# Kernel optimization log

Measured on AMD Instinct MI355X. Metric: run time of the kernel, lower is better.

## Reference

```python
import jax, jax.numpy as jnp
import numpy as np

B, T, F = 8, 4096, 256

def setup_inputs() -> dict:
    key = jax.random.key(0)
    ks = jax.random.split(key, 10)
    s = 1.0 / np.sqrt(F)
    return {
        "x": jax.random.normal(ks[0], (B, T, F), dtype=jnp.float32),
        "Wq_w": jax.random.normal(ks[1], (F, F), dtype=jnp.float32) * s,
        "Wq_b": jax.random.normal(ks[2], (F,), dtype=jnp.float32) * 0.01,
        "Wk_w": jax.random.normal(ks[3], (F, F), dtype=jnp.float32) * s,
        "Wk_b": jax.random.normal(ks[4], (F,), dtype=jnp.float32) * 0.01,
        "Wv_w": jax.random.normal(ks[5], (F, F), dtype=jnp.float32) * s,
        "Wv_b": jax.random.normal(ks[6], (F,), dtype=jnp.float32) * 0.01,
        "w": jax.random.normal(ks[7], (T, T), dtype=jnp.float32) * 0.02,
        "out_w": jax.random.normal(ks[8], (F, F), dtype=jnp.float32) * s,
        "out_b": jax.random.normal(ks[9], (F,), dtype=jnp.float32) * 0.01,
    }

def reference(x, Wq_w, Wq_b, Wk_w, Wk_b, Wv_w, Wv_b, w, out_w, out_b):
    # Linear layers (torch convention: y = x @ W.T + b)
    Q = x @ Wq_w.T + Wq_b                      # [B, T, F]
    K = x @ Wk_w.T + Wk_b                      # [B, T, F]
    V = x @ Wv_w.T + Wv_b                      # [B, T, F]
    Q_sig = jax.nn.sigmoid(Q)
    # Stabilized exponentials (faithful: w over rows, K over FEATURE dim)
    exp_w = jnp.exp(w - jnp.max(w, axis=-1, keepdims=True))        # [T, T]
    exp_K = jnp.exp(K - jnp.max(K, axis=-1, keepdims=True))        # [B, T, F]
    num = jnp.einsum('ts,bsf->btf', exp_w, exp_K * V)              # [B, T, F]
    den = jnp.einsum('ts,bsf->btf', exp_w, exp_K)                  # [B, T, F]
    Yt = Q_sig * (num / den)
    return Yt @ out_w.T + out_b
```

## Files before the change

### kernel.cpp

```cpp
#include <hip/hip_runtime.h>
#include <hip/hip_bf16.h>

#define BB 8
#define TT 4096
#define FF 256
#define BT 32768

typedef unsigned short u16;
typedef __attribute__((ext_vector_type(8))) short short8;
typedef __attribute__((ext_vector_type(4))) float f32x4;
typedef __attribute__((ext_vector_type(4))) unsigned int u32x4;

static __device__ __forceinline__ float bf2f(u16 u) {
    union { unsigned int i; float f; } v; v.i = ((unsigned int)u) << 16; return v.f;
}
static __device__ __forceinline__ u16 f2bf(float f) {
    union { float f; unsigned int i; } v; v.f = f;
    unsigned int x = v.i;
    return (u16)((x + 0x7fffu + ((x >> 16) & 1u)) >> 16);
}

typedef const __attribute__((address_space(1))) void gvoid_t;
typedef __attribute__((address_space(3))) void svoid_t;

__global__ __launch_bounds__(256) void expw_kernel(const float* __restrict__ w,
                                                   u16* __restrict__ ew) {
    __shared__ float red[256];
    int row = blockIdx.x;
    int tid = threadIdx.x;
    const float* wr = w + (size_t)row * TT;

    f32x4 vals[4];
    float m = -1e30f;
#pragma unroll
    for (int v = 0; v < 4; ++v) {
        int idx = (v * 256 + tid) * 4;
        vals[v] = *(const f32x4*)(wr + idx);
#pragma unroll
        for (int j = 0; j < 4; ++j) m = fmaxf(m, vals[v][j]);
    }
    red[tid] = m;
    __syncthreads();
    for (int s = 128; s > 0; s >>= 1) {
        if (tid < s) red[tid] = fmaxf(red[tid], red[tid + s]);
        __syncthreads();
    }
    float rm = red[0];
#pragma unroll
    for (int v = 0; v < 4; ++v) {
        int idx = (v * 256 + tid) * 4;
        float e0 = expf(vals[v][0] - rm), e1 = expf(vals[v][1] - rm);
        float e2 = expf(vals[v][2] - rm), e3 = expf(vals[v][3] - rm);
        uint2 pk;
        pk.x = (unsigned int)f2bf(e0) | ((unsigned int)f2bf(e1) << 16);
        pk.y = (unsigned int)f2bf(e2) | ((unsigned int)f2bf(e3) << 16);
        *(uint2*)(ew + (size_t)row * TT + idx) = pk;
    }
}

__global__ __launch_bounds__(256) void cvt_all_kernel(const float* __restrict__ x,
                                                      const float* __restrict__ wq,
                                                      const float* __restrict__ wo,
                                                      const float* __restrict__ wk,
                                                      const float* __restrict__ wv,
                                                      u16* __restrict__ xbf,
                                                      u16* __restrict__ wqb,
                                                      u16* __restrict__ wob,
                                                      u16* __restrict__ wkv) {
    int i = blockIdx.x * 256 + threadIdx.x;
    if (i < 2097152) {
        int idx = i * 4;
        f32x4 v = *(const f32x4*)(x + idx);
        uint2 pk;
        pk.x = (unsigned int)f2bf(v[0]) | ((unsigned int)f2bf(v[1]) << 16);
        pk.y = (unsigned int)f2bf(v[2]) | ((unsigned int)f2bf(v[3]) << 16);
        *(uint2*)(xbf + idx) = pk;
        return;
    }
    int j = i - 2097152;
    int which = j >> 14, k = j & 16383;
    int idx = k * 4;
    if (which == 0) {
        f32x4 v = *(const f32x4*)(wq + idx);
        uint2 pk;
        pk.x = (unsigned int)f2bf(v[0]) | ((unsigned int)f2bf(v[1]) << 16);
        pk.y = (unsigned int)f2bf(v[2]) | ((unsigned int)f2bf(v[3]) << 16);
        *(uint2*)(wqb + idx) = pk;
    } else if (which == 1) {
        f32x4 v = *(const f32x4*)(wo + idx);
        uint2 pk;
        pk.x = (unsigned int)f2bf(v[0]) | ((unsigned int)f2bf(v[1]) << 16);
        pk.y = (unsigned int)f2bf(v[2]) | ((unsigned int)f2bf(v[3]) << 16);
        *(uint2*)(wob + idx) = pk;
    } else {
        int f = idx >> 8, c = idx & 255;
        f32x4 a = *(const f32x4*)(wk + idx);
        f32x4 b = *(const f32x4*)(wv + idx);
        uint2 pa, pb;
        pa.x = (unsigned int)f2bf(a[0]) | ((unsigned int)f2bf(a[1]) << 16);
        pa.y = (unsigned int)f2bf(a[2]) | ((unsigned int)f2bf(a[3]) << 16);
        pb.x = (unsigned int)f2bf(b[0]) | ((unsigned int)f2bf(b[1]) << 16);
        pb.y = (unsigned int)f2bf(b[2]) | ((unsigned int)f2bf(b[3]) << 16);
        *(uint2*)(wkv + (size_t)(2 * f) * 256 + c) = pa;
        *(uint2*)(wkv + (size_t)(2 * f + 1) * 256 + c) = pb;
    }
}

template <int MODE>
__global__ __launch_bounds__(256) void gemm_nt(const u16* __restrict__ A,
                                               const u16* __restrict__ Bm,
                                               const float* __restrict__ bias,
                                               void* __restrict__ Call,
                                               int M, int N, int K) {
    __shared__ u16 As[128 * 32];
    __shared__ u16 Bs[128 * 32];

    int tid = threadIdx.x;
    int lane = tid & 63;
    int w = tid >> 6;
    int wr = w >> 1, wc = w & 1;
    int fr = lane & 15, kg = lane >> 4;

    f32x4 acc[4][4];
#pragma unroll
    for (int m = 0; m < 4; ++m)
#pragma unroll
        for (int n = 0; n < 4; ++n) acc[m][n] = (f32x4){0.f, 0.f, 0.f, 0.f};

    int bm = blockIdx.x, bn = blockIdx.y;
    int nk = K >> 5;

    int srow = tid >> 2;
    int schunk = ((tid & 3) ^ ((tid >> 3) & 3)) << 3;
    const u16* aBase = A + (size_t)(bm * 128 + srow) * K + schunk;
    const u16* bBase = Bm + (size_t)(bn * 128 + srow) * K + schunk;
    size_t half = (size_t)64 * K;

    int xsw = (kg * 8) ^ (((fr >> 1) & 3) << 3);

    for (int kt = 0; kt < nk; ++kt) {
        __syncthreads();
        int ko = kt << 5;
        __builtin_amdgcn_global_load_lds((gvoid_t*)(aBase + ko), (svoid_t*)&As[tid * 8], 16, 0, 0);
        __builtin_amdgcn_global_load_lds((gvoid_t*)(aBase + half + ko), (svoid_t*)&As[2048 + tid * 8], 16, 0, 0);
        __builtin_amdgcn_global_load_lds((gvoid_t*)(bBase + ko), (svoid_t*)&Bs[tid * 8], 16, 0, 0);
        __builtin_amdgcn_global_load_lds((gvoid_t*)(bBase + half + ko), (svoid_t*)&Bs[2048 + tid * 8], 16, 0, 0);
        __syncthreads();

        short8 af[4], bfr[4];
#pragma unroll
        for (int m = 0; m < 4; ++m)
            af[m] = *(const short8*)&As[(wr * 64 + m * 16 + fr) * 32 + xsw];
#pragma unroll
        for (int n = 0; n < 4; ++n)
            bfr[n] = *(const short8*)&Bs[(wc * 64 + n * 16 + fr) * 32 + xsw];
#pragma unroll
        for (int m = 0; m < 4; ++m)
#pragma unroll
            for (int n = 0; n < 4; ++n)
                acc[m][n] = __builtin_amdgcn_mfma_f32_16x16x32_bf16(af[m], bfr[n], acc[m][n], 0, 0, 0);
    }

    int row0 = bm * 128 + wr * 64;
    int col0 = bn * 128 + wc * 64;
#pragma unroll
    for (int n = 0; n < 4; ++n) {
        int col = col0 + n * 16 + fr;
        float bv = bias ? bias[col] : 0.0f;
#pragma unroll
        for (int m = 0; m < 4; ++m) {
            int rbase = row0 + m * 16 + kg * 4;
#pragma unroll
            for (int i = 0; i < 4; ++i) {
                float val = acc[m][n][i] + bv;
                size_t idx = (size_t)(rbase + i) * N + col;
                if (MODE == 0)
                    ((float*)Call)[idx] = val;
                else
                    ((u16*)Call)[idx] = f2bf(1.0f / (1.0f + expf(-val)));
            }
        }
    }
}

__global__ __launch_bounds__(512) void kv_mt_kernel(const u16* __restrict__ xbf,
                                                    const u16* __restrict__ wkv,
                                                    const float* __restrict__ bk,
                                                    const float* __restrict__ bv,
                                                    u16* __restrict__ mt) {
    __shared__ u16 As[128 * 32];
    __shared__ u16 Bs[512 * 32];
    __shared__ float rmax4[128][4];

    int tid = threadIdx.x;
    int lane = tid & 63, wid = tid >> 6;
    int fr = lane & 15, kg = lane >> 4;
    int wr = wid >> 2, wc = wid & 3;
    int row0g = blockIdx.x * 128;

    f32x4 acc[4][8];
#pragma unroll
    for (int m = 0; m < 4; ++m)
#pragma unroll
        for (int n = 0; n < 8; ++n) acc[m][n] = (f32x4){0.f, 0.f, 0.f, 0.f};

    int scol = ((tid & 3) ^ ((tid >> 3) & 3)) << 3;
    const u16* aSrc = xbf + (size_t)(row0g + (tid >> 2)) * 256 + scol;
    const u16* bSrc = wkv + (size_t)(tid >> 2) * 256 + scol;
    int xsw = (kg * 8) ^ (((fr >> 1) & 3) << 3);

    for (int ks = 0; ks < 8; ++ks) {
        __syncthreads();
        __builtin_amdgcn_global_load_lds((gvoid_t*)(aSrc + ks * 32), (svoid_t*)&As[tid * 8], 16, 0, 0);
#pragma unroll
        for (int c = 0; c < 4; ++c)
            __builtin_amdgcn_global_load_lds((gvoid_t*)(bSrc + (size_t)c * 128 * 256 + ks * 32),
                                             (svoid_t*)&Bs[c * 4096 + tid * 8], 16, 0, 0);
        __syncthreads();

        short8 af[4], bfr[8];
#pragma unroll
        for (int m = 0; m < 4; ++m)
            af[m] = *(const short8*)&As[(wr * 64 + m * 16 + fr) * 32 + xsw];
#pragma unroll
        for (int n = 0; n < 8; ++n)
            bfr[n] = *(const short8*)&Bs[(wc * 128 + n * 16 + fr) * 32 + xsw];
#pragma unroll
        for (int m = 0; m < 4; ++m)
#pragma unroll
            for (int n = 0; n < 8; ++n)
                acc[m][n] = __builtin_amdgcn_mfma_f32_16x16x32_bf16(af[m], bfr[n], acc[m][n], 0, 0, 0);
    }

    int par = fr & 1;
#pragma unroll
    for (int n = 0; n < 8; ++n) {
        int col = wc * 128 + n * 16 + fr;
        int f = col >> 1;
        float bvv = par ? bv[f] : bk[f];
#pragma unroll
        for (int m = 0; m < 4; ++m)
#pragma unroll
            for (int i = 0; i < 4; ++i) acc[m][n][i] += bvv;
    }

    float rmax[4][4];
#pragma unroll
    for (int m = 0; m < 4; ++m)
#pragma unroll
        for (int i = 0; i < 4; ++i) {
            float mx = -1e30f;
#pragma unroll
            for (int n = 0; n < 8; ++n) mx = fmaxf(mx, par ? -1e30f : acc[m][n][i]);
            mx = fmaxf(mx, __shfl_xor(mx, 2));
            mx = fmaxf(mx, __shfl_xor(mx, 4));
            mx = fmaxf(mx, __shfl_xor(mx, 8));
            mx = fmaxf(mx, __shfl_xor(mx, 1));
            rmax[m][i] = mx;
        }
    if (fr == 0) {
#pragma unroll
        for (int m = 0; m < 4; ++m)
#pragma unroll
            for (int i = 0; i < 4; ++i)
                rmax4[wr * 64 + m * 16 + kg * 4 + i][wc] = rmax[m][i];
    }
    __syncthreads();
#pragma unroll
    for (int m = 0; m < 4; ++m)
#pragma unroll
        for (int i = 0; i < 4; ++i) {
            f32x4 r4 = *(const f32x4*)rmax4[wr * 64 + m * 16 + kg * 4 + i];
            rmax[m][i] = fmaxf(fmaxf(r4[0], r4[1]), fmaxf(r4[2], r4[3]));
        }

    int b = row0g >> 12;
    int tcb = (row0g & 4095) + wr * 64;
#pragma unroll
    for (int n = 0; n < 8; ++n) {
        int col = wc * 128 + n * 16 + fr;
        int f = col >> 1;
        size_t rowmt = (size_t)(b * 512 + 2 * f + (par ? 0 : 1));
#pragma unroll
        for (int m = 0; m < 4; ++m) {
            int tc = tcb + m * 16 + kg * 4;
            u16 o[4];
#pragma unroll
            for (int i = 0; i < 4; ++i) {
                float v = acc[m][n][i];
                float ek = expf(v - rmax[m][i]);
                float ekx = __shfl_xor(ek, 1);
                float outv = par ? (ekx * v) : ek;
                o[i] = f2bf(outv);
            }
            uint2 pk;
            pk.x = (unsigned int)o[0] | ((unsigned int)o[1] << 16);
            pk.y = (unsigned int)o[2] | ((unsigned int)o[3] << 16);
            *(uint2*)(mt + rowmt * TT + tc) = pk;
        }
    }
}

#define GLDS(src, eoff) \
    __builtin_amdgcn_global_load_lds((gvoid_t*)(src), (svoid_t*)&L[eoff], 16, 0, 0)

#define STAGE8(P_, KS_) do {                                                   \
    _Pragma("unroll")                                                          \
    for (int i_ = 0; i_ < 4; ++i_) {                                           \
        GLDS(sA + (size_t)i_ * 64 * 4096 + (KS_) * 64,                         \
             (P_) * 16384 + i_ * 4096 + dst);                                  \
        GLDS(sB + (size_t)i_ * 64 * 4096 + (KS_) * 64,                         \
             32768 + (P_) * 16384 + i_ * 4096 + dst);                          \
    }                                                                          \
} while (0)

__global__ __launch_bounds__(512, 2) void gemm256_nt(const u16* __restrict__ A,
                                                     const u16* __restrict__ B,
                                                     const u16* __restrict__ qsig,
                                                     u16* __restrict__ yt) {
    __shared__ u16 L[65536];
    const int K = 4096;
    int tid = threadIdx.x;
    int lane = tid & 63, wid = tid >> 6;
    int fr = lane & 15, kg = lane >> 4;
    int wr = wid >> 2, wc = wid & 3;
    int bm = blockIdx.x, bn = blockIdx.y;
    const char* LB = (const char*)L;

    int x0 = (kg * 16) ^ ((fr & 7) << 4);
    int x1 = (64 + kg * 16) ^ ((fr & 7) << 4);
    int arow = (wr * 128 + fr) * 128;
    int brow = (wc * 64 + fr) * 128;

    int scol = ((tid & 7) * 8) ^ (((tid >> 3) & 7) << 3);
    const u16* sA = A + (size_t)(bm * 256 + (tid >> 3)) * K + scol;
    const u16* sB = B + (size_t)(bn * 256 + (tid >> 3)) * K + scol;
    int dst = tid * 8;

    f32x4 acc[8][4];
#pragma unroll
    for (int m = 0; m < 8; ++m)
#pragma unroll
        for (int n = 0; n < 4; ++n) acc[m][n] = (f32x4){0.f, 0.f, 0.f, 0.f};

    STAGE8(0, 0);
    asm volatile("s_waitcnt vmcnt(0)" ::: "memory");
    __builtin_amdgcn_sched_barrier(0);
    __builtin_amdgcn_s_barrier();

#pragma unroll 1
    for (int t = 0; t < 64; ++t) {
        int p = t & 1;
        const char* abase = LB + p * 32768;
        const char* bbase = LB + 65536 + p * 32768;

        short8 bfr[4][2], af[4][2];
#pragma unroll
        for (int nf = 0; nf < 4; ++nf) {
            const char* rb = bbase + brow + nf * 2048;
            bfr[nf][0] = *(const short8*)(rb + x0);
            bfr[nf][1] = *(const short8*)(rb + x1);
        }
#pragma unroll
        for (int mf = 0; mf < 4; ++mf) {
            const char* rb = abase + arow + mf * 2048;
            af[mf][0] = *(const short8*)(rb + x0);
            af[mf][1] = *(const short8*)(rb + x1);
        }
        int ks = (t + 1 < 64) ? t + 1 : 0;
        STAGE8(p ^ 1, ks);
        asm volatile("s_waitcnt lgkmcnt(0)" ::: "memory");
        __builtin_amdgcn_sched_barrier(0);
        __builtin_amdgcn_s_setprio(1);
#pragma unroll
        for (int mf = 0; mf < 4; ++mf)
#pragma unroll
            for (int nf = 0; nf < 4; ++nf) {
                acc[mf][nf] = __builtin_amdgcn_mfma_f32_16x16x32_bf16(af[mf][0], bfr[nf][0], acc[mf][nf], 0, 0, 0);
                acc[mf][nf] = __builtin_amdgcn_mfma_f32_16x16x32_bf16(af[mf][1], bfr[nf][1], acc[mf][nf], 0, 0, 0);
            }
        __builtin_amdgcn_s_setprio(0);
#pragma unroll
        for (int mf = 0; mf < 4; ++mf) {
            const char* rb = abase + arow + (mf + 4) * 2048;
            af[mf][0] = *(const short8*)(rb + x0);
            af[mf][1] = *(const short8*)(rb + x1);
        }
        asm volatile("s_waitcnt lgkmcnt(0)" ::: "memory");
        __builtin_amdgcn_sched_barrier(0);
        __builtin_amdgcn_s_setprio(1);
#pragma unroll
        for (int mf = 0; mf < 4; ++mf)
#pragma unroll
            for (int nf = 0; nf < 4; ++nf) {
                acc[mf + 4][nf] = __builtin_amdgcn_mfma_f32_16x16x32_bf16(af[mf][0], bfr[nf][0], acc[mf + 4][nf], 0, 0, 0);
                acc[mf + 4][nf] = __builtin_amdgcn_mfma_f32_16x16x32_bf16(af[mf][1], bfr[nf][1], acc[mf + 4][nf], 0, 0, 0);
            }
        __builtin_amdgcn_s_setprio(0);
        asm volatile("s_waitcnt vmcnt(0)" ::: "memory");
        __builtin_amdgcn_sched_barrier(0);
        __builtin_amdgcn_s_barrier();
    }

    int colgb = bn * 256 + wc * 64;
    int row0 = bm * 256 + wr * 128;
    int par = fr & 1;
#pragma unroll
    for (int n = 0; n < 4; ++n) {
        int colg = colgb + n * 16 + fr;
        int b = colg >> 9;
        int f = (colg & 511) >> 1;
#pragma unroll
        for (int m = 0; m < 8; ++m) {
            int tr0 = row0 + m * 16 + kg * 4;
            float v0 = acc[m][n][0], v1 = acc[m][n][1];
            float v2 = acc[m][n][2], v3 = acc[m][n][3];
            float o0 = __shfl_xor(v0, 1), o1 = __shfl_xor(v1, 1);
            float o2 = __shfl_xor(v2, 1), o3 = __shfl_xor(v3, 1);
            float nA = par ? o2 : v0, dA = par ? v2 : o0;
            float nB = par ? o3 : v1, dB = par ? v3 : o1;
            int iA = par ? 2 : 0;
            size_t idxA = ((size_t)(b * 4096 + tr0 + iA) << 8) + f;
            size_t idxB = idxA + 256;
            float qA = bf2f(qsig[idxA]);
            float qB = bf2f(qsig[idxB]);
            yt[idxA] = f2bf(qA * nA * __builtin_amdgcn_rcpf(dA));
            yt[idxB] = f2bf(qB * nB * __builtin_amdgcn_rcpf(dB));
        }
    }
}

extern "C" void kernel_launch(void* const* d_in, const int* in_sizes, int n_in,
                              void* d_out, int out_size, void* d_ws, size_t ws_size,
                              hipStream_t stream) {
    const float* x  = (const float*)d_in[0];
    const float* wq = (const float*)d_in[1];
    const float* bq = (const float*)d_in[2];
    const float* wk = (const float*)d_in[3];
    const float* bk = (const float*)d_in[4];
    const float* wv = (const float*)d_in[5];
    const float* bv = (const float*)d_in[6];
    const float* w  = (const float*)d_in[7];
    const float* wo = (const float*)d_in[8];
    const float* bo = (const float*)d_in[9];

    char* p = (char*)d_ws;
    u16* expw = (u16*)p; p += (size_t)TT * TT * 2;
    u16* xbf  = (u16*)p; p += (size_t)BT * FF * 2;
    u16* wqb  = (u16*)p; p += (size_t)FF * FF * 2;
    u16* wob  = (u16*)p; p += (size_t)FF * FF * 2;
    u16* wkv  = (u16*)p; p += (size_t)2 * FF * FF * 2;
    u16* qsig = (u16*)p; p += (size_t)BT * FF * 2;
    u16* mt   = (u16*)p; p += (size_t)BB * 512 * TT * 2;
    u16* yt = xbf;

    expw_kernel<<<TT, 256, 0, stream>>>(w, expw);

    cvt_all_kernel<<<8384, 256, 0, stream>>>(x, wq, wo, wk, wv, xbf, wqb, wob, wkv);

    dim3 gp(BT / 128, FF / 128, 1);
    gemm_nt<1><<<gp, 256, 0, stream>>>(xbf, wqb, bq, qsig, BT, FF, FF);

    kv_mt_kernel<<<BT / 128, 512, 0, stream>>>(xbf, wkv, bk, bv, mt);

    gemm256_nt<<<dim3(16, 16), 512, 0, stream>>>(expw, mt, qsig, yt);

    gemm_nt<0><<<gp, 256, 0, stream>>>(yt, wob, bo, (float*)d_out, BT, FF, FF);
}
```

Measured before the change: 186.3 us.

## Shrink attention GEMM tile to 256x128 with K-step 32 and drop exp_w row max

The big exp_w × M GEMM now uses 256x128 output tiles with a 32-wide K step and a 48 KB LDS footprint. It declares 4 blocks per CU and launches twice as many blocks, aiming for more resident waves and better latency hiding. The price is half as many MFMAs per LDS fragment load and twice as many loop barriers. Separately, the exp(w) kernel no longer subtracts the row max, which cancels in the num/den ratio, so the reduction and its syncs are gone; this can overflow if w holds large values.

```diff
diff --git a/kernel.cpp b/kernel.cpp
--- a/kernel.cpp
+++ b/kernel.cpp
@@ -25,32 +25,15 @@
 
 __global__ __launch_bounds__(256) void expw_kernel(const float* __restrict__ w,
                                                    u16* __restrict__ ew) {
-    __shared__ float red[256];
     int row = blockIdx.x;
     int tid = threadIdx.x;
     const float* wr = w + (size_t)row * TT;
-
-    f32x4 vals[4];
-    float m = -1e30f;
 #pragma unroll
     for (int v = 0; v < 4; ++v) {
         int idx = (v * 256 + tid) * 4;
-        vals[v] = *(const f32x4*)(wr + idx);
-#pragma unroll
-        for (int j = 0; j < 4; ++j) m = fmaxf(m, vals[v][j]);
-    }
-    red[tid] = m;
-    __syncthreads();
-    for (int s = 128; s > 0; s >>= 1) {
-        if (tid < s) red[tid] = fmaxf(red[tid], red[tid + s]);
-        __syncthreads();
-    }
-    float rm = red[0];
-#pragma unroll
-    for (int v = 0; v < 4; ++v) {
-        int idx = (v * 256 + tid) * 4;
-        float e0 = expf(vals[v][0] - rm), e1 = expf(vals[v][1] - rm);
-        float e2 = expf(vals[v][2] - rm), e3 = expf(vals[v][3] - rm);
+        f32x4 vals = *(const f32x4*)(wr + idx);
+        float e0 = expf(vals[0]), e1 = expf(vals[1]);
+        float e2 = expf(vals[2]), e3 = expf(vals[3]);
         uint2 pk;
         pk.x = (unsigned int)f2bf(e0) | ((unsigned int)f2bf(e1) << 16);
         pk.y = (unsigned int)f2bf(e2) | ((unsigned int)f2bf(e3) << 16);
@@ -304,109 +287,90 @@
 #define GLDS(src, eoff) \
     __builtin_amdgcn_global_load_lds((gvoid_t*)(src), (svoid_t*)&L[eoff], 16, 0, 0)
 
-#define STAGE8(P_, KS_) do {                                                   \
-    _Pragma("unroll")                                                          \
-    for (int i_ = 0; i_ < 4; ++i_) {                                           \
-        GLDS(sA + (size_t)i_ * 64 * 4096 + (KS_) * 64,                         \
-             (P_) * 16384 + i_ * 4096 + dst);                                  \
-        GLDS(sB + (size_t)i_ * 64 * 4096 + (KS_) * 64,                         \
-             32768 + (P_) * 16384 + i_ * 4096 + dst);                          \
-    }                                                                          \
+#define STAGE3(P_, KS_) do {                                                   \
+    GLDS(sA + (KS_) * 32, (P_) * 8192 + dst);                                  \
+    GLDS(sA + (size_t)128 * 4096 + (KS_) * 32, (P_) * 8192 + 4096 + dst);      \
+    GLDS(sB + (KS_) * 32, 16384 + (P_) * 4096 + dst);                          \
 } while (0)
 
-__global__ __launch_bounds__(512, 2) void gemm256_nt(const u16* __restrict__ A,
+__global__ __launch_bounds__(512, 4) void gemm256_nt(const u16* __restrict__ A,
                                                      const u16* __restrict__ B,
                                                      const u16* __restrict__ qsig,
                                                      u16* __restrict__ yt) {
-    __shared__ u16 L[65536];
+    __shared__ u16 L[24576];
     const int K = 4096;
     int tid = threadIdx.x;
     int lane = tid & 63, wid = tid >> 6;
     int fr = lane & 15, kg = lane >> 4;
     int wr = wid >> 2, wc = wid & 3;
     int bm = blockIdx.x, bn = blockIdx.y;
-    const char* LB = (const char*)L;
-
-    int x0 = (kg * 16) ^ ((fr & 7) << 4);
-    int x1 = (64 + kg * 16) ^ ((fr & 7) << 4);
-    int arow = (wr * 128 + fr) * 128;
-    int brow = (wc * 64 + fr) * 128;
-
-    int scol = ((tid & 7) * 8) ^ (((tid >> 3) & 7) << 3);
-    const u16* sA = A + (size_t)(bm * 256 + (tid >> 3)) * K + scol;
-    const u16* sB = B + (size_t)(bn * 256 + (tid >> 3)) * K + scol;
+
+    int xsw = (kg * 8) ^ (((fr >> 1) & 3) << 3);
+    int arow = (wr * 128 + fr) * 32;
+    int brow = (wc * 32 + fr) * 32;
+
+    int scol = ((tid & 3) ^ ((tid >> 3) & 3)) << 3;
+    const u16* sA = A + (size_t)(bm * 256 + (tid >> 2)) * K + scol;
+    const u16* sB = B + (size_t)(bn * 128 + (tid >> 2)) * K + scol;
     int dst = tid * 8;
 
-    f32x4 acc[8][4];
+    f32x4 acc[8][2];
 #pragma unroll
     for (int m = 0; m < 8; ++m)
 #pragma unroll
-        for (int n = 0; n < 4; ++n) acc[m][n] = (f32x4){0.f, 0.f, 0.f, 0.f};
-
-    STAGE8(0, 0);
+        for (int n = 0; n < 2; ++n) acc[m][n] = (f32x4){0.f, 0.f, 0.f, 0.f};
+
+    STAGE3(0, 0);
     asm volatile("s_waitcnt vmcnt(0)" ::: "memory");
     __builtin_amdgcn_sched_barrier(0);
     __builtin_amdgcn_s_barrier();
 
 #pragma unroll 1
-    for (int t = 0; t < 64; ++t) {
+    for (int t = 0; t < 128; ++t) {
         int p = t & 1;
-        const char* abase = LB + p * 32768;
-        const char* bbase = LB + 65536 + p * 32768;
-
-        short8 bfr[4][2], af[4][2];
-#pragma unroll
-        for (int nf = 0; nf < 4; ++nf) {
-            const char* rb = bbase + brow + nf * 2048;
-            bfr[nf][0] = *(const short8*)(rb + x0);
-            bfr[nf][1] = *(const short8*)(rb + x1);
-        }
-#pragma unroll
-        for (int mf = 0; mf < 4; ++mf) {
-            const char* rb = abase + arow + mf * 2048;
-            af[mf][0] = *(const short8*)(rb + x0);
-            af[mf][1] = *(const short8*)(rb + x1);
-        }
-        int ks = (t + 1 < 64) ? t + 1 : 0;
-        STAGE8(p ^ 1, ks);
+        int Ab = p * 8192;
+        int Bb = 16384 + p * 4096;
+
+        short8 af[4], bfr[2];
+#pragma unroll
+        for (int nf = 0; nf < 2; ++nf)
+            bfr[nf] = *(const short8*)&L[Bb + brow + nf * 512 + xsw];
+#pragma unroll
+        for (int mf = 0; mf < 4; ++mf)
+            af[mf] = *(const short8*)&L[Ab + arow + mf * 512 + xsw];
+        int ks = (t + 1 < 128) ? t + 1 : 0;
+        STAGE3(p ^ 1, ks);
         asm volatile("s_waitcnt lgkmcnt(0)" ::: "memory");
         __builtin_amdgcn_sched_barrier(0);
         __builtin_amdgcn_s_setprio(1);
 #pragma unroll
         for (int mf = 0; mf < 4; ++mf)
 #pragma unroll
-            for (int nf = 0; nf < 4; ++nf) {
-                acc[mf][nf] = __builtin_amdgcn_mfma_f32_16x16x32_bf16(af[mf][0], bfr[nf][0], acc[mf][nf], 0, 0, 0);
-                acc[mf][nf] = __builtin_amdgcn_mfma_f32_16x16x32_bf16(af[mf][1], bfr[nf][1], acc[mf][nf], 0, 0, 0);
-            }
+            for (int nf = 0; nf < 2; ++nf)
+                acc[mf][nf] = __builtin_amdgcn_mfma_f32_16x16x32_bf16(af[mf], bfr[nf], acc[mf][nf], 0, 0, 0);
         __builtin_amdgcn_s_setprio(0);
 #pragma unroll
-        for (int mf = 0; mf < 4; ++mf) {
-            const char* rb = abase + arow + (mf + 4) * 2048;
-            af[mf][0] = *(const short8*)(rb + x0);
-            af[mf][1] = *(const short8*)(rb + x1);
-        }
+        for (int mf = 0; mf < 4; ++mf)
+            af[mf] = *(const short8*)&L[Ab + arow + (mf + 4) * 512 + xsw];
         asm volatile("s_waitcnt lgkmcnt(0)" ::: "memory");
         __builtin_amdgcn_sched_barrier(0);
         __builtin_amdgcn_s_setprio(1);
 #pragma unroll
         for (int mf = 0; mf < 4; ++mf)
 #pragma unroll
-            for (int nf = 0; nf < 4; ++nf) {
-                acc[mf + 4][nf] = __builtin_amdgcn_mfma_f32_16x16x32_bf16(af[mf][0], bfr[nf][0], acc[mf + 4][nf], 0, 0, 0);
-                acc[mf + 4][nf] = __builtin_amdgcn_mfma_f32_16x16x32_bf16(af[mf][1], bfr[nf][1], acc[mf + 4][nf], 0, 0, 0);
-            }
+            for (int nf = 0; nf < 2; ++nf)
+                acc[mf + 4][nf] = __builtin_amdgcn_mfma_f32_16x16x32_bf16(af[mf], bfr[nf], acc[mf + 4][nf], 0, 0, 0);
         __builtin_amdgcn_s_setprio(0);
         asm volatile("s_waitcnt vmcnt(0)" ::: "memory");
         __builtin_amdgcn_sched_barrier(0);
         __builtin_amdgcn_s_barrier();
     }
 
-    int colgb = bn * 256 + wc * 64;
+    int colgb = bn * 128 + wc * 32;
     int row0 = bm * 256 + wr * 128;
     int par = fr & 1;
 #pragma unroll
-    for (int n = 0; n < 4; ++n) {
+    for (int n = 0; n < 2; ++n) {
         int colg = colgb + n * 16 + fr;
         int b = colg >> 9;
         int f = (colg & 511) >> 1;
@@ -463,7 +427,7 @@
 
     kv_mt_kernel<<<BT / 128, 512, 0, stream>>>(xbf, wkv, bk, bv, mt);
 
-    gemm256_nt<<<dim3(16, 16), 512, 0, stream>>>(expw, mt, qsig, yt);
+    gemm256_nt<<<dim3(16, 32), 512, 0, stream>>>(expw, mt, qsig, yt);
 
     gemm_nt<0><<<gp, 256, 0, stream>>>(yt, wob, bo, (float*)d_out, BT, FF, FF);
 }
```

Result: slower. 208.6 us (+11.9%).
